# Kernel optimization log

Measured on AMD Instinct MI355X. Metric: run time of the kernel, lower is better.

Reference implementation:

```python
import jax, jax.numpy as jnp
import numpy as np

EMBED_DIM = 512
NHEAD = 8
HEAD_DIM = EMBED_DIM // NHEAD
NEG_INF = -1e8
U, B, R, S, M = 1024, 16, 256, 32, 31
Q = R + U + S   # 1312
KV = M + R + U  # 1311


def setup_inputs() -> dict:
    key = jax.random.key(0)
    ks = jax.random.split(key, 12)
    f = lambda k, shp: jax.random.normal(k, shp, dtype=jnp.float32)
    s = 1.0 / np.sqrt(EMBED_DIM)
    return {
        "utterance": f(ks[0], (U, B, EMBED_DIM)),
        "right_context": f(ks[1], (R, B, EMBED_DIM)),
        "summary": f(ks[2], (S, B, EMBED_DIM)),
        "memory": f(ks[3], (M, B, EMBED_DIM)),
        "attention_mask": jax.random.randint(ks[4], (Q, KV), 0, 2).astype(bool),
        "padding_mask": jax.random.randint(ks[5], (B, KV), 0, 2).astype(bool),
        "Wq": f(ks[6], (EMBED_DIM, EMBED_DIM)) * s,
        "bq": f(ks[7], (EMBED_DIM,)) * 0.1,
        "Wkv": f(ks[8], (2 * EMBED_DIM, EMBED_DIM)) * s,
        "bkv": f(ks[9], (2 * EMBED_DIM,)) * 0.1,
        "Wo": f(ks[10], (EMBED_DIM, EMBED_DIM)) * s * 0.25,
        "bo": f(ks[11], (EMBED_DIM,)) * 0.1,
    }


def reference(utterance, right_context, summary, memory, attention_mask,
              padding_mask, Wq, bq, Wkv, bkv, Wo, bo):
    scaling = HEAD_DIM ** -0.5
    # query = [right_context, utterance, summary]  -> (Q, B, D)
    q_in = jnp.concatenate([right_context, utterance, summary], axis=0)
    # key/value = [memory, right_context, utterance] -> (KV, B, D)
    kv_in = jnp.concatenate([memory, right_context, utterance], axis=0)
    query = q_in @ Wq.T + bq
    kv = kv_in @ Wkv.T + bkv
    key_t, value = jnp.split(kv, 2, axis=2)

    def heads(t):  # (L, B, D) -> (B*nhead, L, head_dim)
        return t.reshape(t.shape[0], B * NHEAD, HEAD_DIM).transpose(1, 0, 2)

    qh = heads(query) * scaling
    kh = heads(key_t)
    vh = heads(value)
    # (B*nhead, Q, KV) attention scores in float32 (matches .float() cast)
    w = jnp.einsum('bqd,bkd->bqk', qh, kh).astype(jnp.float32)
    w = jnp.where(attention_mask[None], NEG_INF, w)
    w = w.reshape(B, NHEAD, Q, KV)
    w = jnp.where(padding_mask[:, None, None, :], NEG_INF, w)
    probs = jax.nn.softmax(w.reshape(B * NHEAD, Q, KV), axis=-1)
    # dropout p=0.0 -> identity
    attn = jnp.einsum('bqk,bkd->bqd', probs, vh)  # (B*nhead, Q, head_dim)
    attn = attn.transpose(1, 0, 2).reshape(Q, B, EMBED_DIM)
    out = attn @ Wo.T + bo
    output_right_context_utterance = out[:R + U]
    # tanh_on_mem=False -> clamp to [-10, 10]; forward returns memory[:-1]
    output_memory = jnp.clip(out[R + U:], -10.0, 10.0)[:-1]
    return output_right_context_utterance, output_memory
```

## Files before the change

kernel.cpp:

```cpp
#include <hip/hip_runtime.h>
#include <hip/hip_bf16.h>

#define EMBED 512
#define NHEAD 8
#define HDIM  64
#define B_    16
#define U_    1024
#define R_    256
#define S_    32
#define M_    31
#define Q_    (R_ + U_ + S_)
#define KV_   (M_ + R_ + U_)

#define QROWS  (Q_ * B_)
#define KVROWS (KV_ * B_)
#define OROWS  (1311 * B_)
#define OUT0_ROWS (1280 * B_)

#define KVPAD_ROWS 1408
#define KPAD 1408
#define MROWSTRIDE 44

#define QSCALE 0.18033688011112042f
#define SOFFI (-16.0f)
#define MASKV (-56.0f)

typedef __attribute__((ext_vector_type(8))) short bf16x8;
typedef __attribute__((ext_vector_type(4))) short short4v;
typedef __attribute__((ext_vector_type(4))) float f32x4;
#define MFMA16(a, b, c) __builtin_amdgcn_mfma_f32_16x16x32_bf16(a, b, c, 0, 0, 0)

typedef unsigned short ushort_t;

__device__ __forceinline__ ushort_t f2bf(float x) {
    __hip_bfloat16 h = __float2bfloat16(x);
    return *reinterpret_cast<ushort_t*>(&h);
}
__device__ __forceinline__ float bf2f(ushort_t h) {
    return __uint_as_float((unsigned)h << 16);
}
__device__ __forceinline__ float exp2_raw(float x) {
    return __builtin_amdgcn_exp2f(x);
}

__device__ __forceinline__ void gload_lds16(const void* g, void* l) {
    __builtin_amdgcn_global_load_lds(
        (const __attribute__((address_space(1))) unsigned int*)g,
        (__attribute__((address_space(3))) unsigned int*)l, 16, 0, 0);
}

__global__ __launch_bounds__(256) void cvt_all(
    const float* __restrict__ s0, const float* __restrict__ s1,
    const float* __restrict__ s2, const float* __restrict__ s3,
    const float* __restrict__ s4, const float* __restrict__ s5,
    const float* __restrict__ s6,
    ushort_t* __restrict__ SRC_hi, ushort_t* __restrict__ W_hi,
    const int* __restrict__ am, const int* __restrict__ pm,
    unsigned* __restrict__ am_p, unsigned* __restrict__ pm_p)
{
    int bid = blockIdx.x;
    if (bid >= 5884) {
        const int NA = Q_ * MROWSTRIDE;
        const int NP = B_ * MROWSTRIDE;
        int idx = (bid - 5884) * 256 + threadIdx.x;
        if (idx < NA) {
            int q = idx / MROWSTRIDE, w_ = idx % MROWSTRIDE;
            unsigned bits = 0xFFFFFFFFu;
            if (w_ < 41) {
                bits = 0;
                #pragma unroll 4
                for (int i = 0; i < 32; ++i) {
                    int kg = w_ * 32 + i;
                    int v = (kg < KV_) ? am[(size_t)q * KV_ + kg] : 1;
                    bits |= (unsigned)(v != 0) << i;
                }
            }
            am_p[idx] = bits;
        } else if (idx < NA + NP) {
            int j = idx - NA;
            int bb = j / MROWSTRIDE, w_ = j % MROWSTRIDE;
            unsigned bits = 0xFFFFFFFFu;
            if (w_ < 41) {
                bits = 0;
                #pragma unroll 4
                for (int i = 0; i < 32; ++i) {
                    int kg = w_ * 32 + i;
                    int v = (kg < KV_) ? pm[bb * KV_ + kg] : 1;
                    bits |= (unsigned)(v != 0) << i;
                }
            }
            pm_p[j] = bits;
        }
        return;
    }

    const float* src; ushort_t* hi; int n8;
    if (bid < 4096)      { src = s0; hi = SRC_hi;            n8 = 1048576; }
    else if (bid < 5120) { src = s1; hi = SRC_hi + 8388608;  n8 = 262144; bid -= 4096; }
    else if (bid < 5248) { src = s2; hi = SRC_hi + 10485760; n8 = 32768;  bid -= 5120; }
    else if (bid < 5372) { src = s3; hi = SRC_hi + 10747904; n8 = 31744;  bid -= 5248; }
    else if (bid < 5500) { src = s4; hi = W_hi;              n8 = 32768;  bid -= 5372; }
    else if (bid < 5756) { src = s5; hi = W_hi + 262144;     n8 = 65536;  bid -= 5500; }
    else                 { src = s6; hi = W_hi + 786432;     n8 = 32768;  bid -= 5756; }

    int i = bid * 256 + threadIdx.x;
    if (i >= n8) return;
    const float4* s = (const float4*)(src + (size_t)i * 8);
    float4 a = s[0], b2 = s[1];
    float xs[8] = {a.x, a.y, a.z, a.w, b2.x, b2.y, b2.z, b2.w};
    bf16x8 hv;
    #pragma unroll
    for (int j = 0; j < 8; ++j) hv[j] = (short)f2bf(xs[j]);
    *(bf16x8*)(hi + (size_t)i * 8) = hv;
}

__global__ __launch_bounds__(256) void vtrans(
    const ushort_t* __restrict__ Vp, ushort_t* __restrict__ VT)
{
    __shared__ ushort_t Lt[64][72];
    const int tid = threadIdx.x;
    const int kt  = blockIdx.x;
    const int bh  = blockIdx.y;
    const int b   = bh >> 3, h = bh & 7;
    const int sub = tid >> 3;
    const int g   = tid & 7;

    #pragma unroll
    for (int p = 0; p < 2; ++p) {
        int k = kt * 64 + p * 32 + sub;
        bf16x8 v;
        if (k < KV_) {
            v = *(const bf16x8*)(Vp + ((size_t)k * B_ + b) * EMBED + h * HDIM + g * 8);
        } else {
            #pragma unroll
            for (int j = 0; j < 8; ++j) v[j] = 0;
        }
        #pragma unroll
        for (int j = 0; j < 8; ++j)
            Lt[g * 8 + j][p * 32 + sub] = (ushort_t)v[j];
    }
    __syncthreads();
    #pragma unroll
    for (int p = 0; p < 2; ++p) {
        int d = p * 32 + sub;
        bf16x8 v = *(const bf16x8*)&Lt[d][g * 8];
        if (d & 8) {
            bf16x8 t;
            #pragma unroll
            for (int j = 0; j < 8; ++j) t[j] = v[j ^ 4];
            v = t;
        }
        *(bf16x8*)(VT + ((size_t)(bh * 64 + d)) * KPAD + kt * 64 + g * 8) = v;
    }
}

template<int MODE>
__global__ __launch_bounds__(256) void gemm_mfma(
    const ushort_t* __restrict__ A, const ushort_t* __restrict__ W,
    const float* __restrict__ bias, float scale,
    int n0, int n01, int nrows,
    size_t off0, size_t off1, size_t off2,
    void* __restrict__ o0, void* __restrict__ o1, void* __restrict__ o2)
{
    __shared__ __align__(16) ushort_t lA[128][64];
    __shared__ __align__(16) ushort_t lW[128][64];

    const int tid = threadIdx.x;
    const int w   = tid >> 6;
    const int l   = tid & 63;
    const int l15 = l & 15;
    const int l4  = l >> 4;
    const int row0 = blockIdx.x * 128;
    const int col0 = blockIdx.y * 128;

    const int drow = l >> 3;
    const int sgr  = (l & 7) ^ drow;
    const ushort_t* aptr[4];
    const ushort_t* wptr[4];
    #pragma unroll
    for (int c = 0; c < 4; ++c) {
        int r = row0 + w * 32 + c * 8 + drow;
        int rc = r < nrows ? r : nrows - 1;
        size_t roff;
        if (MODE == 2)      roff = (size_t)rc * EMBED;
        else if (rc < n0)   roff = off0 + (size_t)rc * EMBED;
        else if (rc < n01)  roff = off1 + (size_t)(rc - n0) * EMBED;
        else                roff = off2 + (size_t)(rc - n01) * EMBED;
        aptr[c] = A + roff + sgr * 8;
        int wr = col0 + w * 32 + c * 8 + drow;
        wptr[c] = W + (size_t)wr * EMBED + sgr * 8;
    }

    f32x4 acc[4][4];
    #pragma unroll
    for (int mi = 0; mi < 4; ++mi)
        #pragma unroll
        for (int nj = 0; nj < 4; ++nj) acc[mi][nj] = (f32x4){0.f, 0.f, 0.f, 0.f};

    const int wrow = (w >> 1) * 64;
    const int wcol = (w & 1) * 64;

    for (int t = 0; t < 8; ++t) {
        __syncthreads();
        const int ke = t * 64;
        #pragma unroll
        for (int c = 0; c < 4; ++c) {
            gload_lds16(aptr[c] + ke, &lA[w * 32 + c * 8][0]);
            gload_lds16(wptr[c] + ke, &lW[w * 32 + c * 8][0]);
        }
        __syncthreads();

        #pragma unroll
        for (int kk = 0; kk < 2; ++kk) {
            bf16x8 ah[4], wh[4];
            #pragma unroll
            for (int mi = 0; mi < 4; ++mi) {
                int row = wrow + mi * 16 + l15;
                int g = (((kk * 4 + l4) ^ (l15 & 7))) * 8;
                ah[mi] = *(const bf16x8*)&lA[row][g];
            }
            #pragma unroll
            for (int nj = 0; nj < 4; ++nj) {
                int row = wcol + nj * 16 + l15;
                int g = (((kk * 4 + l4) ^ (l15 & 7))) * 8;
                wh[nj] = *(const bf16x8*)&lW[row][g];
            }
            #pragma unroll
            for (int mi = 0; mi < 4; ++mi)
                #pragma unroll
                for (int nj = 0; nj < 4; ++nj)
                    acc[mi][nj] = MFMA16(ah[mi], wh[nj], acc[mi][nj]);
        }
    }

    #pragma unroll
    for (int nj = 0; nj < 4; ++nj) {
        int gc = col0 + wcol + nj * 16 + l15;
        float bv = bias[gc];
        #pragma unroll
        for (int mi = 0; mi < 4; ++mi) {
            #pragma unroll
            for (int r = 0; r < 4; ++r) {
                int gr = row0 + wrow + mi * 16 + l4 * 4 + r;
                if (gr >= nrows) continue;
                float v = (acc[mi][nj][r] + bv) * scale;
                if (MODE == 0) {
                    ((ushort_t*)o0)[(size_t)gr * EMBED + gc] = f2bf(v);
                } else if (MODE == 1) {
                    if (gc < EMBED)
                        ((ushort_t*)o0)[(size_t)gr * EMBED + gc] = f2bf(v);
                    else
                        ((ushort_t*)o2)[(size_t)gr * EMBED + (gc - EMBED)] = f2bf(v);
                } else {
                    if (gr < OUT0_ROWS)
                        ((float*)o0)[(size_t)gr * EMBED + gc] = v;
                    else if (gr < OROWS)
                        ((float*)o1)[(size_t)(gr - OUT0_ROWS) * EMBED + gc] =
                            fminf(fmaxf(v, -10.f), 10.f);
                }
            }
        }
    }
}

__global__ __launch_bounds__(512, 4) void attn_mfma(
    const ushort_t* __restrict__ Q_p,
    const ushort_t* __restrict__ Khi_p, const ushort_t* __restrict__ VT,
    const unsigned* __restrict__ am_p, const unsigned* __restrict__ pm_p,
    ushort_t* __restrict__ C_p)
{
    __shared__ __align__(16) ushort_t SM[32768];
    #define KlAt(buf, row) (SM + (buf) * 8192 + (row) * 64)
    #define VtAt(buf, row) (SM + 16384 + (buf) * 8192 + (row) * 128)

    const int tid = threadIdx.x;
    const int w   = tid >> 6;
    const int l   = tid & 63;
    const int l15 = l & 15;
    const int l4  = l >> 4;
    const int q0  = blockIdx.x * 128;
    const int bh  = blockIdx.y;
    const int b   = bh >> 3, h = bh & 7;

    bf16x8 Qf[2];
    {
        int qa = q0 + w * 16 + l15;
        if (qa >= Q_) qa = Q_ - 1;
        size_t base = ((size_t)qa * B_ + b) * EMBED + h * HDIM;
        #pragma unroll
        for (int dh = 0; dh < 2; ++dh)
            Qf[dh] = *(const bf16x8*)(Q_p + base + dh * 32 + l4 * 8);
    }

    bf16x8 ONES;
    #pragma unroll
    for (int j = 0; j < 8; ++j) ONES[j] = (l15 == 0) ? (short)0x3F80 : (short)0;

    const unsigned* awp;
    {
        int q = q0 + w * 16 + l15;
        if (q >= Q_) q = Q_ - 1;
        awp = am_p + (size_t)q * MROWSTRIDE;
    }
    const unsigned* pwp = pm_p + b * MROWSTRIDE;

    const int krl = l >> 3;
    const int gsK = (l & 7) ^ krl;
    const ushort_t* kSrc0 =
        Khi_p + ((size_t)(w * 8 + krl) * B_ + b) * EMBED + h * HDIM + gsK * 8;

    const int vro = l >> 4;
    const int g16 = l & 15;
    const ushort_t* vSrcA =
        VT + ((size_t)(bh * 64 + w * 8 + vro)) * KPAD + ((g16 ^ vro) * 8);
    const ushort_t* vSrcB =
        VT + ((size_t)(bh * 64 + w * 8 + 4 + vro)) * KPAD + ((g16 ^ (4 + vro)) * 8);

    const int gb  = l4 >> 1;
    const int hsw = ((l4 & 1) ^ ((l15 >> 3) & 1)) * 4;
    const int x7  = l15 & 7;

    f32x4 SS = (f32x4){0.f, 0.f, 0.f, 0.f};
    f32x4 O[4];
    #pragma unroll
    for (int dg = 0; dg < 4; ++dg) O[dg] = (f32x4){0.f, 0.f, 0.f, 0.f};

    auto stage = [&](int kbase, int buf) {
        gload_lds16(kSrc0 + (size_t)kbase * B_ * EMBED,        KlAt(buf, w * 8));
        gload_lds16(kSrc0 + (size_t)(kbase + 64) * B_ * EMBED, KlAt(buf, 64 + w * 8));
        gload_lds16(vSrcA + kbase, VtAt(buf, w * 8));
        gload_lds16(vSrcB + kbase, VtAt(buf, w * 8 + 4));
    };

    stage(0, 0);
    __syncthreads();
    int cur = 0;

    for (int kt = 0; kt < 11; ++kt) {
        uint2 pw0 = *(const uint2*)&pwp[4 * kt];
        uint2 pw1 = *(const uint2*)&pwp[4 * kt + 2];
        uint2 aw0 = *(const uint2*)&awp[4 * kt];
        uint2 aw1 = *(const uint2*)&awp[4 * kt + 2];
        unsigned mm[4];
        mm[0] = (aw0.x | pw0.x) >> (l4 * 4);
        mm[1] = (aw0.y | pw0.y) >> (l4 * 4);
        mm[2] = (aw1.x | pw1.x) >> (l4 * 4);
        mm[3] = (aw1.y | pw1.y) >> (l4 * 4);

        if (kt < 10) stage((kt + 1) * 128, cur ^ 1);

        f32x4 S[8];
        __builtin_amdgcn_s_setprio(1);
        #pragma unroll
        for (int c = 0; c < 8; ++c) {
            f32x4 acc = (f32x4){SOFFI, SOFFI, SOFFI, SOFFI};
            int krow = c * 16 + l15;
            #pragma unroll
            for (int dh = 0; dh < 2; ++dh) {
                int gr = ((dh * 4 + l4) ^ x7) * 8;
                bf16x8 Bh = *(const bf16x8*)(KlAt(cur, krow) + gr);
                acc = MFMA16(Bh, Qf[dh], acc);
            }
            S[c] = acc;
        }
        __builtin_amdgcn_s_setprio(0);

        bf16x8 PB[4];
        #pragma unroll
        for (int c = 0; c < 8; ++c) {
            unsigned mw = mm[c >> 1];
            int sh = (c & 1) << 4;
            #pragma unroll
            for (int r = 0; r < 4; ++r) {
                float s = ((mw >> (sh + r)) & 1) ? MASKV : S[c][r];
                PB[c >> 1][(c & 1) * 4 + r] = (short)f2bf(exp2_raw(s));
            }
        }

        __builtin_amdgcn_s_setprio(1);
        SS = MFMA16(ONES, PB[0], SS);
        SS = MFMA16(ONES, PB[1], SS);
        SS = MFMA16(ONES, PB[2], SS);
        SS = MFMA16(ONES, PB[3], SS);
        #pragma unroll
        for (int kh = 0; kh < 4; ++kh) {
            #pragma unroll
            for (int dg = 0; dg < 4; ++dg) {
                int rw = dg * 16 + l15;
                const ushort_t* vrow = VtAt(cur, rw);
                int G0 = (kh * 4 + gb) ^ x7;
                int G1 = (kh * 4 + 2 + gb) ^ x7;
                union { bf16x8 v8; short4v h2[2]; } u;
                u.h2[0] = *(const short4v*)(vrow + G0 * 8 + hsw);
                u.h2[1] = *(const short4v*)(vrow + G1 * 8 + hsw);
                O[dg] = MFMA16(u.v8, PB[kh], O[dg]);
            }
        }
        __builtin_amdgcn_s_setprio(0);

        __syncthreads();
        cur ^= 1;
    }

    float sT  = __shfl(SS[0], l15, 64);
    float inv = 1.f / sT;

    float* TB = ((float*)SM) + w * 1024;
    #pragma unroll
    for (int dg = 0; dg < 4; ++dg) {
        f32x4 vv;
        #pragma unroll
        for (int r = 0; r < 4; ++r) vv[r] = O[dg][r] * inv;
        int gsw = (dg * 4 + l4) ^ (l15 & 7);
        *(f32x4*)(TB + l15 * 64 + gsw * 4) = vv;
    }

    #pragma unroll
    for (int qq = 0; qq < 16; ++qq) {
        int q = q0 + w * 16 + qq;
        if (q >= Q_) break;
        float v = TB[qq * 64 + (((l >> 2) ^ (qq & 7)) * 4) + (l & 3)];
        size_t off = ((size_t)q * B_ + b) * EMBED + h * HDIM + l;
        C_p[off] = f2bf(v);
    }
    #undef KlAt
    #undef VtAt
}

extern "C" void kernel_launch(void* const* d_in, const int* in_sizes, int n_in,
                              void* d_out, int out_size, void* d_ws, size_t ws_size,
                              hipStream_t stream) {
    const float* utter = (const float*)d_in[0];
    const float* rctx  = (const float*)d_in[1];
    const float* summ  = (const float*)d_in[2];
    const float* mem   = (const float*)d_in[3];
    const int* amask   = (const int*)d_in[4];
    const int* pmask   = (const int*)d_in[5];
    const float* Wq  = (const float*)d_in[6];
    const float* bq  = (const float*)d_in[7];
    const float* Wkv = (const float*)d_in[8];
    const float* bkv = (const float*)d_in[9];
    const float* Wo  = (const float*)d_in[10];
    const float* bo  = (const float*)d_in[11];

    const size_t UT_OFF = 0;
    const size_t RC_OFF = 8388608;
    const size_t SM_OFF = 10485760;
    const size_t MM_OFF = 10747904;
    const size_t SRC_N  = 11001856;
    const size_t WQ_OFF = 0, WKV_OFF = 262144, WO_OFF = 786432;
    const size_t W_N = 1048576;
    const size_t KVPLANE = (size_t)KVPAD_ROWS * B_ * EMBED;

    ushort_t* p = (ushort_t*)d_ws;
    ushort_t* SRC_hi = p;                p += SRC_N;
    ushort_t* Wp_hi  = p;                p += W_N;
    ushort_t* Q_p    = p;                p += (size_t)QROWS * EMBED;
    ushort_t* Khi_p  = p;                p += KVPLANE;
    ushort_t* VT_p   = p;                p += KVPLANE;
    ushort_t* Vp     = p;                p += KVPLANE;
    ushort_t* C_p    = p;                p += (size_t)QROWS * EMBED;
    unsigned* am_p   = (unsigned*)p;     p += (size_t)2 * KVPAD_ROWS * MROWSTRIDE;
    unsigned* pm_p   = (unsigned*)p;     p += (size_t)2 * B_ * MROWSTRIDE;

    float* out0 = (float*)d_out;
    float* out1 = out0 + (size_t)OUT0_ROWS * EMBED;

    dim3 blk(256);

    cvt_all<<<dim3(6113), blk, 0, stream>>>(
        utter, rctx, summ, mem, Wq, Wkv, Wo,
        SRC_hi, Wp_hi, amask, pmask, am_p, pm_p);

    gemm_mfma<0><<<dim3(QROWS / 128, EMBED / 128), blk, 0, stream>>>(
        SRC_hi, Wp_hi + WQ_OFF, bq, QSCALE,
        R_ * B_, (R_ + U_) * B_, QROWS, RC_OFF, UT_OFF, SM_OFF,
        Q_p, nullptr, nullptr);

    gemm_mfma<1><<<dim3((KVROWS + 127) / 128, (2 * EMBED) / 128), blk, 0, stream>>>(
        SRC_hi, Wp_hi + WKV_OFF, bkv, 1.0f,
        M_ * B_, (M_ + R_) * B_, KVROWS, MM_OFF, RC_OFF, UT_OFF,
        Khi_p, nullptr, Vp);

    vtrans<<<dim3(22, 128), blk, 0, stream>>>(Vp, VT_p);

    attn_mfma<<<dim3((Q_ + 127) / 128, B_ * NHEAD), dim3(512), 0, stream>>>(
        Q_p, Khi_p, VT_p, am_p, pm_p, C_p);

    gemm_mfma<2><<<dim3(QROWS / 128, EMBED / 128), blk, 0, stream>>>(
        C_p, Wp_hi + WO_OFF, bo, 1.0f,
        QROWS, QROWS, QROWS, 0, 0, 0,
        out0, out1, nullptr);
}
```

Baseline: 285.1 us.

## Fuse Q projection GEMM with V transpose and skip inactive query waves

Merges the Q-projection GEMM and the V transpose into one launch: the first 656 blocks compute Q and the rest transpose V, so one kernel launch and its tail disappear and the two independent jobs can overlap. The Q GEMM runs after the KV GEMM now. In attention, waves whose 16 query rows lie beyond Q skip mask loads, MFMAs and exp work but keep taking part in the barriers, and they return before the epilogue. The risks are some wasted shared memory for transpose blocks and uneven block sizes inside the fused launch.

```diff
diff --git a/kernel.cpp b/kernel.cpp
--- a/kernel.cpp
+++ b/kernel.cpp
@@ -114,46 +114,6 @@
     *(bf16x8*)(hi + (size_t)i * 8) = hv;
 }
 
-__global__ __launch_bounds__(256) void vtrans(
-    const ushort_t* __restrict__ Vp, ushort_t* __restrict__ VT)
-{
-    __shared__ ushort_t Lt[64][72];
-    const int tid = threadIdx.x;
-    const int kt  = blockIdx.x;
-    const int bh  = blockIdx.y;
-    const int b   = bh >> 3, h = bh & 7;
-    const int sub = tid >> 3;
-    const int g   = tid & 7;
-
-    #pragma unroll
-    for (int p = 0; p < 2; ++p) {
-        int k = kt * 64 + p * 32 + sub;
-        bf16x8 v;
-        if (k < KV_) {
-            v = *(const bf16x8*)(Vp + ((size_t)k * B_ + b) * EMBED + h * HDIM + g * 8);
-        } else {
-            #pragma unroll
-            for (int j = 0; j < 8; ++j) v[j] = 0;
-        }
-        #pragma unroll
-        for (int j = 0; j < 8; ++j)
-            Lt[g * 8 + j][p * 32 + sub] = (ushort_t)v[j];
-    }
-    __syncthreads();
-    #pragma unroll
-    for (int p = 0; p < 2; ++p) {
-        int d = p * 32 + sub;
-        bf16x8 v = *(const bf16x8*)&Lt[d][g * 8];
-        if (d & 8) {
-            bf16x8 t;
-            #pragma unroll
-            for (int j = 0; j < 8; ++j) t[j] = v[j ^ 4];
-            v = t;
-        }
-        *(bf16x8*)(VT + ((size_t)(bh * 64 + d)) * KPAD + kt * 64 + g * 8) = v;
-    }
-}
-
 template<int MODE>
 __global__ __launch_bounds__(256) void gemm_mfma(
     const ushort_t* __restrict__ A, const ushort_t* __restrict__ W,
@@ -244,9 +204,7 @@
                 int gr = row0 + wrow + mi * 16 + l4 * 4 + r;
                 if (gr >= nrows) continue;
                 float v = (acc[mi][nj][r] + bv) * scale;
-                if (MODE == 0) {
-                    ((ushort_t*)o0)[(size_t)gr * EMBED + gc] = f2bf(v);
-                } else if (MODE == 1) {
+                if (MODE == 1) {
                     if (gc < EMBED)
                         ((ushort_t*)o0)[(size_t)gr * EMBED + gc] = f2bf(v);
                     else
@@ -263,6 +221,140 @@
     }
 }
 
+__global__ __launch_bounds__(256) void fuse_q_vt(
+    const ushort_t* __restrict__ SRC, const ushort_t* __restrict__ Wq,
+    const float* __restrict__ bq,
+    const ushort_t* __restrict__ Vp,
+    ushort_t* __restrict__ Q_p, ushort_t* __restrict__ VT)
+{
+    __shared__ __align__(16) ushort_t SMEM[16384];
+    const int tid = threadIdx.x;
+
+    if (blockIdx.x >= 656) {
+        int b2 = blockIdx.x - 656;
+        const int kt = b2 % 22;
+        const int bh = b2 / 22;
+        const int b  = bh >> 3, h = bh & 7;
+        const int sub = tid >> 3;
+        const int g   = tid & 7;
+        ushort_t (*Lt)[72] = (ushort_t(*)[72])SMEM;
+
+        #pragma unroll
+        for (int p = 0; p < 2; ++p) {
+            int k = kt * 64 + p * 32 + sub;
+            bf16x8 v;
+            if (k < KV_) {
+                v = *(const bf16x8*)(Vp + ((size_t)k * B_ + b) * EMBED + h * HDIM + g * 8);
+            } else {
+                #pragma unroll
+                for (int j = 0; j < 8; ++j) v[j] = 0;
+            }
+            #pragma unroll
+            for (int j = 0; j < 8; ++j)
+                Lt[g * 8 + j][p * 32 + sub] = (ushort_t)v[j];
+        }
+        __syncthreads();
+        #pragma unroll
+        for (int p = 0; p < 2; ++p) {
+            int d = p * 32 + sub;
+            bf16x8 v = *(const bf16x8*)&Lt[d][g * 8];
+            if (d & 8) {
+                bf16x8 t;
+                #pragma unroll
+                for (int j = 0; j < 8; ++j) t[j] = v[j ^ 4];
+                v = t;
+            }
+            *(bf16x8*)(VT + ((size_t)(bh * 64 + d)) * KPAD + kt * 64 + g * 8) = v;
+        }
+        return;
+    }
+
+    ushort_t* lA = SMEM;
+    ushort_t* lW = SMEM + 8192;
+
+    const int w   = tid >> 6;
+    const int l   = tid & 63;
+    const int l15 = l & 15;
+    const int l4  = l >> 4;
+    const int row0 = (blockIdx.x >> 2) * 128;
+    const int col0 = (blockIdx.x & 3) * 128;
+
+    const int drow = l >> 3;
+    const int sgr  = (l & 7) ^ drow;
+    const ushort_t* aptr[4];
+    const ushort_t* wptr[4];
+    #pragma unroll
+    for (int c = 0; c < 4; ++c) {
+        int r = row0 + w * 32 + c * 8 + drow;
+        int rc = r < QROWS ? r : QROWS - 1;
+        size_t roff;
+        if (rc < R_ * B_)              roff = (size_t)8388608  + (size_t)rc * EMBED;
+        else if (rc < (R_ + U_) * B_)  roff = (size_t)(rc - R_ * B_) * EMBED;
+        else                           roff = (size_t)10485760 + (size_t)(rc - (R_ + U_) * B_) * EMBED;
+        aptr[c] = SRC + roff + sgr * 8;
+        int wr = col0 + w * 32 + c * 8 + drow;
+        wptr[c] = Wq + (size_t)wr * EMBED + sgr * 8;
+    }
+
+    f32x4 acc[4][4];
+    #pragma unroll
+    for (int mi = 0; mi < 4; ++mi)
+        #pragma unroll
+        for (int nj = 0; nj < 4; ++nj) acc[mi][nj] = (f32x4){0.f, 0.f, 0.f, 0.f};
+
+    const int wrow = (w >> 1) * 64;
+    const int wcol = (w & 1) * 64;
+
+    for (int t = 0; t < 8; ++t) {
+        __syncthreads();
+        const int ke = t * 64;
+        #pragma unroll
+        for (int c = 0; c < 4; ++c) {
+            gload_lds16(aptr[c] + ke, lA + (w * 32 + c * 8) * 64);
+            gload_lds16(wptr[c] + ke, lW + (w * 32 + c * 8) * 64);
+        }
+        __syncthreads();
+
+        #pragma unroll
+        for (int kk = 0; kk < 2; ++kk) {
+            bf16x8 ah[4], wh[4];
+            #pragma unroll
+            for (int mi = 0; mi < 4; ++mi) {
+                int row = wrow + mi * 16 + l15;
+                int g = (((kk * 4 + l4) ^ (l15 & 7))) * 8;
+                ah[mi] = *(const bf16x8*)(lA + row * 64 + g);
+            }
+            #pragma unroll
+            for (int nj = 0; nj < 4; ++nj) {
+                int row = wcol + nj * 16 + l15;
+                int g = (((kk * 4 + l4) ^ (l15 & 7))) * 8;
+                wh[nj] = *(const bf16x8*)(lW + row * 64 + g);
+            }
+            #pragma unroll
+            for (int mi = 0; mi < 4; ++mi)
+                #pragma unroll
+                for (int nj = 0; nj < 4; ++nj)
+                    acc[mi][nj] = MFMA16(ah[mi], wh[nj], acc[mi][nj]);
+        }
+    }
+
+    #pragma unroll
+    for (int nj = 0; nj < 4; ++nj) {
+        int gc = col0 + wcol + nj * 16 + l15;
+        float bv = bq[gc];
+        #pragma unroll
+        for (int mi = 0; mi < 4; ++mi) {
+            #pragma unroll
+            for (int r = 0; r < 4; ++r) {
+                int gr = row0 + wrow + mi * 16 + l4 * 4 + r;
+                if (gr >= QROWS) continue;
+                float v = (acc[mi][nj][r] + bv) * QSCALE;
+                Q_p[(size_t)gr * EMBED + gc] = f2bf(v);
+            }
+        }
+    }
+}
+
 __global__ __launch_bounds__(512, 4) void attn_mfma(
     const ushort_t* __restrict__ Q_p,
     const ushort_t* __restrict__ Khi_p, const ushort_t* __restrict__ VT,
@@ -281,6 +373,7 @@
     const int q0  = blockIdx.x * 128;
     const int bh  = blockIdx.y;
     const int b   = bh >> 3, h = bh & 7;
+    const bool qact = (q0 + w * 16) < Q_;
 
     bf16x8 Qf[2];
     {
@@ -337,71 +430,74 @@
     int cur = 0;
 
     for (int kt = 0; kt < 11; ++kt) {
-        uint2 pw0 = *(const uint2*)&pwp[4 * kt];
-        uint2 pw1 = *(const uint2*)&pwp[4 * kt + 2];
-        uint2 aw0 = *(const uint2*)&awp[4 * kt];
-        uint2 aw1 = *(const uint2*)&awp[4 * kt + 2];
-        unsigned mm[4];
-        mm[0] = (aw0.x | pw0.x) >> (l4 * 4);
-        mm[1] = (aw0.y | pw0.y) >> (l4 * 4);
-        mm[2] = (aw1.x | pw1.x) >> (l4 * 4);
-        mm[3] = (aw1.y | pw1.y) >> (l4 * 4);
-
         if (kt < 10) stage((kt + 1) * 128, cur ^ 1);
 
-        f32x4 S[8];
-        __builtin_amdgcn_s_setprio(1);
-        #pragma unroll
-        for (int c = 0; c < 8; ++c) {
-            f32x4 acc = (f32x4){SOFFI, SOFFI, SOFFI, SOFFI};
-            int krow = c * 16 + l15;
-            #pragma unroll
-            for (int dh = 0; dh < 2; ++dh) {
-                int gr = ((dh * 4 + l4) ^ x7) * 8;
-                bf16x8 Bh = *(const bf16x8*)(KlAt(cur, krow) + gr);
-                acc = MFMA16(Bh, Qf[dh], acc);
-            }
-            S[c] = acc;
-        }
-        __builtin_amdgcn_s_setprio(0);
-
-        bf16x8 PB[4];
-        #pragma unroll
-        for (int c = 0; c < 8; ++c) {
-            unsigned mw = mm[c >> 1];
-            int sh = (c & 1) << 4;
-            #pragma unroll
-            for (int r = 0; r < 4; ++r) {
-                float s = ((mw >> (sh + r)) & 1) ? MASKV : S[c][r];
-                PB[c >> 1][(c & 1) * 4 + r] = (short)f2bf(exp2_raw(s));
-            }
-        }
-
-        __builtin_amdgcn_s_setprio(1);
-        SS = MFMA16(ONES, PB[0], SS);
-        SS = MFMA16(ONES, PB[1], SS);
-        SS = MFMA16(ONES, PB[2], SS);
-        SS = MFMA16(ONES, PB[3], SS);
-        #pragma unroll
-        for (int kh = 0; kh < 4; ++kh) {
-            #pragma unroll
-            for (int dg = 0; dg < 4; ++dg) {
-                int rw = dg * 16 + l15;
-                const ushort_t* vrow = VtAt(cur, rw);
-                int G0 = (kh * 4 + gb) ^ x7;
-                int G1 = (kh * 4 + 2 + gb) ^ x7;
-                union { bf16x8 v8; short4v h2[2]; } u;
-                u.h2[0] = *(const short4v*)(vrow + G0 * 8 + hsw);
-                u.h2[1] = *(const short4v*)(vrow + G1 * 8 + hsw);
-                O[dg] = MFMA16(u.v8, PB[kh], O[dg]);
-            }
-        }
-        __builtin_amdgcn_s_setprio(0);
+        if (qact) {
+            uint2 pw0 = *(const uint2*)&pwp[4 * kt];
+            uint2 pw1 = *(const uint2*)&pwp[4 * kt + 2];
+            uint2 aw0 = *(const uint2*)&awp[4 * kt];
+            uint2 aw1 = *(const uint2*)&awp[4 * kt + 2];
+            unsigned mm[4];
+            mm[0] = (aw0.x | pw0.x) >> (l4 * 4);
+            mm[1] = (aw0.y | pw0.y) >> (l4 * 4);
+            mm[2] = (aw1.x | pw1.x) >> (l4 * 4);
+            mm[3] = (aw1.y | pw1.y) >> (l4 * 4);
+
+            f32x4 S[8];
+            __builtin_amdgcn_s_setprio(1);
+            #pragma unroll
+            for (int c = 0; c < 8; ++c) {
+                f32x4 acc = (f32x4){SOFFI, SOFFI, SOFFI, SOFFI};
+                int krow = c * 16 + l15;
+                #pragma unroll
+                for (int dh = 0; dh < 2; ++dh) {
+                    int gr = ((dh * 4 + l4) ^ x7) * 8;
+                    bf16x8 Bh = *(const bf16x8*)(KlAt(cur, krow) + gr);
+                    acc = MFMA16(Bh, Qf[dh], acc);
+                }
+                S[c] = acc;
+            }
+            __builtin_amdgcn_s_setprio(0);
+
+            bf16x8 PB[4];
+            #pragma unroll
+            for (int c = 0; c < 8; ++c) {
+                unsigned mw = mm[c >> 1];
+                int sh = (c & 1) << 4;
+                #pragma unroll
+                for (int r = 0; r < 4; ++r) {
+                    float s = ((mw >> (sh + r)) & 1) ? MASKV : S[c][r];
+                    PB[c >> 1][(c & 1) * 4 + r] = (short)f2bf(exp2_raw(s));
+                }
+            }
+
+            __builtin_amdgcn_s_setprio(1);
+            SS = MFMA16(ONES, PB[0], SS);
+            SS = MFMA16(ONES, PB[1], SS);
+            SS = MFMA16(ONES, PB[2], SS);
+            SS = MFMA16(ONES, PB[3], SS);
+            #pragma unroll
+            for (int kh = 0; kh < 4; ++kh) {
+                #pragma unroll
+                for (int dg = 0; dg < 4; ++dg) {
+                    int rw = dg * 16 + l15;
+                    const ushort_t* vrow = VtAt(cur, rw);
+                    int G0 = (kh * 4 + gb) ^ x7;
+                    int G1 = (kh * 4 + 2 + gb) ^ x7;
+                    union { bf16x8 v8; short4v h2[2]; } u;
+                    u.h2[0] = *(const short4v*)(vrow + G0 * 8 + hsw);
+                    u.h2[1] = *(const short4v*)(vrow + G1 * 8 + hsw);
+                    O[dg] = MFMA16(u.v8, PB[kh], O[dg]);
+                }
+            }
+            __builtin_amdgcn_s_setprio(0);
+        }
 
         __syncthreads();
         cur ^= 1;
     }
 
+    if (!qact) return;
     float sT  = __shfl(SS[0], l15, 64);
     float inv = 1.f / sT;
 
@@ -472,17 +568,13 @@
         utter, rctx, summ, mem, Wq, Wkv, Wo,
         SRC_hi, Wp_hi, amask, pmask, am_p, pm_p);
 
-    gemm_mfma<0><<<dim3(QROWS / 128, EMBED / 128), blk, 0, stream>>>(
-        SRC_hi, Wp_hi + WQ_OFF, bq, QSCALE,
-        R_ * B_, (R_ + U_) * B_, QROWS, RC_OFF, UT_OFF, SM_OFF,
-        Q_p, nullptr, nullptr);
-
     gemm_mfma<1><<<dim3((KVROWS + 127) / 128, (2 * EMBED) / 128), blk, 0, stream>>>(
         SRC_hi, Wp_hi + WKV_OFF, bkv, 1.0f,
         M_ * B_, (M_ + R_) * B_, KVROWS, MM_OFF, RC_OFF, UT_OFF,
         Khi_p, nullptr, Vp);
 
-    vtrans<<<dim3(22, 128), blk, 0, stream>>>(Vp, VT_p);
+    fuse_q_vt<<<dim3(656 + 22 * 128), blk, 0, stream>>>(
+        SRC_hi, Wp_hi + WQ_OFF, bq, Vp, Q_p, VT_p);
 
     attn_mfma<<<dim3((Q_ + 127) / 128, B_ * NHEAD), dim3(512), 0, stream>>>(
         Q_p, Khi_p, VT_p, am_p, pm_p, C_p);
```

New measurement: 276.4 us. 1.03x faster.
